# Kernel optimization log

Hardware: AMD Instinct MI355X
Metric: run time of the kernel (lower is better)

## Reference

```python
import jax, jax.numpy as jnp
import numpy as np
import math

D_MODEL = 1024
NUM_HEADS = 16
HEAD_DIM = D_MODEL // NUM_HEADS
B, L = 4, 1024


def setup_inputs() -> dict:
    key = jax.random.key(0)
    ks = jax.random.split(key, 14)
    s = 1.0 / math.sqrt(D_MODEL)
    return {
        "q": jax.random.normal(ks[0], (B, L, D_MODEL), jnp.float32),
        "k": jax.random.normal(ks[1], (B, L, D_MODEL), jnp.float32),
        "v": jax.random.normal(ks[2], (B, L, D_MODEL), jnp.float32),
        "Wq": jax.random.normal(ks[3], (D_MODEL, D_MODEL), jnp.float32) * s,
        "bq": jnp.zeros((D_MODEL,), jnp.float32),
        "Wk": jax.random.normal(ks[4], (D_MODEL, D_MODEL), jnp.float32) * s,
        "bk": jnp.zeros((D_MODEL,), jnp.float32),
        "Wv": jax.random.normal(ks[5], (D_MODEL, D_MODEL), jnp.float32) * s,
        "bv": jnp.zeros((D_MODEL,), jnp.float32),
        "Wo": jax.random.normal(ks[6], (D_MODEL, D_MODEL), jnp.float32) * s,
        "bo": jnp.zeros((D_MODEL,), jnp.float32),
        "lambda_q": jax.random.normal(ks[7], (HEAD_DIM,), jnp.float32) * 0.1,
        "lambda_k": jax.random.normal(ks[8], (HEAD_DIM,), jnp.float32) * 0.1,
        "lambda_v": jax.random.normal(ks[9], (HEAD_DIM,), jnp.float32) * 0.1,
    }


def reference(q, k, v, Wq, bq, Wk, bk, Wv, bv, Wo, bo, lambda_q, lambda_k, lambda_v):
    Bq, Lq, _ = q.shape
    # projections (torch Linear: x @ W.T + b)
    def split_heads(x):
        return x.reshape(Bq, -1, NUM_HEADS, HEAD_DIM).transpose(0, 2, 1, 3)  # [B,H,L,hd]
    qh = split_heads(q @ Wq.T + bq)
    kh = split_heads(k @ Wk.T + bk)
    vh = split_heads(v @ Wv.T + bv)

    lam_self = jnp.exp(jnp.sum(lambda_q * lambda_k))
    lam_cross = jnp.exp(jnp.sum(lambda_k * lambda_v))
    scale = 1.0 / math.sqrt(HEAD_DIM)

    scores_self = jnp.einsum('bhld,bhmd->bhlm', kh, vh) * scale   # [B,H,Lk,Lk]
    scores_cross = jnp.einsum('bhld,bhmd->bhlm', qh, kh) * scale  # [B,H,Lq,Lk]
    scores = scores_cross * lam_cross + scores_self * lam_self

    attn_weights = jax.nn.softmax(jnp.nan_to_num(scores, nan=0.0), axis=-1)
    attn_out = jnp.einsum('bhlm,bhmd->bhld', attn_weights, vh)
    attn_out = attn_out.transpose(0, 2, 1, 3).reshape(Bq, Lq, D_MODEL)
    out = attn_out @ Wo.T + bo
    return (out, attn_weights)
```

## Files before the change

### kernel.cpp

```cpp
#include <hip/hip_runtime.h>
#include <math.h>

#define D_MODEL 1024
#define NHEADS  16
#define HD      64
#define BSZ     4
#define LSEQ    1024
#define BH      64

typedef _Float16 f16;
typedef _Float16 f16x8 __attribute__((ext_vector_type(8)));
typedef _Float16 f16x4 __attribute__((ext_vector_type(4)));
typedef float    f32x4 __attribute__((ext_vector_type(4)));

typedef const __attribute__((address_space(1))) void* gp1_t;
typedef __attribute__((address_space(3))) void* lp3_t;

__device__ __forceinline__ void gload_lds16(const void* g, void* l) {
    __builtin_amdgcn_global_load_lds((gp1_t)g, (lp3_t)l, 16, 0, 0);
}

__global__ void lam_kernel(const float* __restrict__ lq, const float* __restrict__ lk,
                           const float* __restrict__ lv, float* __restrict__ lam) {
    int t = threadIdx.x;
    float pc = lk[t] * lv[t];
    float ps = lq[t] * lk[t];
#pragma unroll
    for (int o = 32; o > 0; o >>= 1) {
        pc += __shfl_down(pc, o, 64);
        ps += __shfl_down(ps, o, 64);
    }
    if (t == 0) {
        float lamC = expf(pc), lamS = expf(ps);
        lam[0] = lamC; lam[1] = lamS;
        lam[2] = lamC / lamS;
        lam[3] = 0.125f * lamS;
    }
}

__global__ void cvt_f32_f16_kernel(const float* __restrict__ src, f16* __restrict__ dst, int n8) {
    int i = blockIdx.x * blockDim.x + threadIdx.x;
    if (i < n8) {
        float4 a = *(const float4*)(src + (size_t)i * 8);
        float4 b = *(const float4*)(src + (size_t)i * 8 + 4);
        f16x8 h;
        h[0]=(f16)a.x; h[1]=(f16)a.y; h[2]=(f16)a.z; h[3]=(f16)a.w;
        h[4]=(f16)b.x; h[5]=(f16)b.y; h[6]=(f16)b.z; h[7]=(f16)b.w;
        *(f16x8*)(dst + (size_t)i * 8) = h;
    }
}

template<int AMODE, int OMODE>
__global__ __launch_bounds__(256) void gemm16_kernel(
    const void* __restrict__ Aarg, const f16* __restrict__ B16,
    const float* __restrict__ bias, const float* __restrict__ lam,
    void* __restrict__ Yarg)
{
    __shared__ f16 At[128 * 64];
    __shared__ f16 Btl[128 * 64];

    const int t = threadIdx.x;
    const int lane = t & 63, w = t >> 6;
    const int g = lane >> 4, ln = lane & 15;
    const int wr = w >> 1, wc = w & 1;
    const int n0 = blockIdx.x * 128, m0 = blockIdx.y * 128;

    f32x4 acc[4][4];
#pragma unroll
    for (int mi = 0; mi < 4; ++mi)
#pragma unroll
        for (int ni = 0; ni < 4; ++ni)
            acc[mi][ni] = (f32x4){0.f, 0.f, 0.f, 0.f};

    for (int kt = 0; kt < 16; ++kt) {
        if (AMODE == 0) {
            const float* X = (const float*)Aarg;
            int r = t >> 1, k0 = (t & 1) * 32;
            const float* src = X + (size_t)(m0 + r) * 1024 + kt * 64 + k0;
#pragma unroll
            for (int c = 0; c < 4; ++c) {
                float4 f0 = *(const float4*)(src + c * 8);
                float4 f1 = *(const float4*)(src + c * 8 + 4);
                f16x8 hv;
                hv[0]=(f16)f0.x; hv[1]=(f16)f0.y; hv[2]=(f16)f0.z; hv[3]=(f16)f0.w;
                hv[4]=(f16)f1.x; hv[5]=(f16)f1.y; hv[6]=(f16)f1.z; hv[7]=(f16)f1.w;
                int kb = (k0 + c * 8) * 2;
                *(f16x8*)((char*)At + r * 128 + (kb ^ ((r & 7) << 4))) = hv;
            }
        } else {
            const f16* A16 = (const f16*)Aarg;
#pragma unroll
            for (int i = 0; i < 4; ++i) {
                int o = t * 16 + i * 4096;
                int r = o >> 7, kb = (o & 127) ^ ((r & 7) << 4);
                gload_lds16(A16 + (size_t)(m0 + r) * 1024 + kt * 64 + (kb >> 1), (char*)At + o);
            }
        }
#pragma unroll
        for (int i = 0; i < 4; ++i) {
            int o = t * 16 + i * 4096;
            int r = o >> 7, kb = (o & 127) ^ ((r & 7) << 4);
            gload_lds16(B16 + (size_t)(n0 + r) * 1024 + kt * 64 + (kb >> 1), (char*)Btl + o);
        }
        __syncthreads();
#pragma unroll
        for (int ks = 0; ks < 2; ++ks) {
            f16x8 af[4], bf[4];
#pragma unroll
            for (int mi = 0; mi < 4; ++mi) {
                int r = wr * 64 + mi * 16 + ln;
                af[mi] = *(const f16x8*)((const char*)At + r * 128 + ((ks * 64 + g * 16) ^ ((r & 7) << 4)));
            }
#pragma unroll
            for (int ni = 0; ni < 4; ++ni) {
                int r = wc * 64 + ni * 16 + ln;
                bf[ni] = *(const f16x8*)((const char*)Btl + r * 128 + ((ks * 64 + g * 16) ^ ((r & 7) << 4)));
            }
#pragma unroll
            for (int mi = 0; mi < 4; ++mi)
#pragma unroll
                for (int ni = 0; ni < 4; ++ni)
                    acc[mi][ni] = __builtin_amdgcn_mfma_f32_16x16x32_f16(af[mi], bf[ni], acc[mi][ni], 0, 0, 0);
        }
        __syncthreads();
    }

    float alpha = 1.0f;
    if (OMODE == 1) alpha = lam[2];
#pragma unroll
    for (int mi = 0; mi < 4; ++mi) {
#pragma unroll
        for (int ni = 0; ni < 4; ++ni) {
            int n = n0 + wc * 64 + ni * 16 + ln;
            float bn = bias[n];
#pragma unroll
            for (int q = 0; q < 4; ++q) {
                int m = m0 + wr * 64 + mi * 16 + 4 * g + q;
                float v = acc[mi][ni][q] + bn;
                if (OMODE == 0) {
                    ((float*)Yarg)[(size_t)m * 1024 + n] = v;
                } else {
                    v *= alpha;
                    int b = m >> 10, l = m & 1023;
                    int h = n >> 6, d = n & 63;
                    ((f16*)Yarg)[(((size_t)(b * NHEADS + h)) * LSEQ + l) * HD + d] = (f16)v;
                }
            }
        }
    }
}

__global__ __launch_bounds__(256) void vtrans_kernel(const f16* __restrict__ Vh, f16* __restrict__ Vt) {
    __shared__ f16 tile[64 * 72];
    int t = threadIdx.x;
    int cb = blockIdx.x;
    int bh = blockIdx.y;
    size_t base = (size_t)bh * LSEQ * HD;
    {
        int c = t >> 2, d0 = (t & 3) * 16;
        f16x8 v0 = *(const f16x8*)(Vh + base + (size_t)(cb * 64 + c) * HD + d0);
        f16x8 v1 = *(const f16x8*)(Vh + base + (size_t)(cb * 64 + c) * HD + d0 + 8);
        *(f16x8*)((char*)tile + c * 144 + d0 * 2) = v0;
        *(f16x8*)((char*)tile + c * 144 + d0 * 2 + 16) = v1;
    }
    __syncthreads();
    {
        int d = t >> 2, c0 = (t & 3) * 16;
        f16 buf[16];
#pragma unroll
        for (int j = 0; j < 16; ++j)
            buf[j] = *(const f16*)((const char*)tile + (c0 + j) * 144 + d * 2);
        f16x8 o0, o1;
#pragma unroll
        for (int j = 0; j < 8; ++j) { o0[j] = buf[j]; o1[j] = buf[j + 8]; }
        size_t ob = (size_t)bh * HD * LSEQ + (size_t)d * LSEQ + cb * 64 + c0;
        *(f16x8*)(Vt + ob) = o0;
        *(f16x8*)(Vt + ob + 8) = o1;
    }
}

__global__ __launch_bounds__(256) void attn_kernel(
    const f16* __restrict__ Qs, const f16* __restrict__ Kh, const f16* __restrict__ Vh,
    const f16* __restrict__ Vt, const float* __restrict__ lam,
    float* __restrict__ attnW, f16* __restrict__ AO)
{
    __shared__ f16 Qt[64 * 128];
    __shared__ f16 Bt[64 * 128];
    __shared__ f16 Vts[64 * 64];
    __shared__ f16 Ws[64 * 72];
    __shared__ float linv[64];

    const int t = threadIdx.x;
    const int lane = t & 63;
    const int w = t >> 6;
    const int g = lane >> 4;
    const int ln = lane & 15;
    const int rb = blockIdx.x;
    const int bh = blockIdx.y;
    const size_t hbase = (size_t)bh * LSEQ * HD;
    const float gamma = lam[3];

    {
        const int r0 = rb * 64;
#pragma unroll
        for (int i = 0; i < 4; ++i) {
            int o = t * 16 + i * 4096;
            int r = o >> 8, kb = (o & 255) ^ ((r & 7) << 4);
            const f16* src = (kb < 128) ? (Qs + hbase + (size_t)(r0 + r) * HD + (kb >> 1))
                                        : (Kh + hbase + (size_t)(r0 + r) * HD + ((kb - 128) >> 1));
            gload_lds16(src, (char*)Qt + o);
        }
    }
    __syncthreads();

    f16x8 qf[4];
    {
        int r = w * 16 + ln;
#pragma unroll
        for (int ks = 0; ks < 4; ++ks)
            qf[ks] = *(const f16x8*)((const char*)Qt + r * 256 + ((ks * 64 + g * 16) ^ ((r & 7) << 4)));
    }

    float lsum = 0.f;
    for (int tt = 0; tt < 16; ++tt) {
        {
            const int c0 = tt * 64;
#pragma unroll
            for (int i = 0; i < 4; ++i) {
                int o = t * 16 + i * 4096;
                int r = o >> 8, kb = (o & 255) ^ ((r & 7) << 4);
                const f16* src = (kb < 128) ? (Kh + hbase + (size_t)(c0 + r) * HD + (kb >> 1))
                                            : (Vh + hbase + (size_t)(c0 + r) * HD + ((kb - 128) >> 1));
                gload_lds16(src, (char*)Bt + o);
            }
        }
        __syncthreads();
#pragma unroll
        for (int ci = 0; ci < 4; ++ci) {
            f32x4 acc = (f32x4){0.f, 0.f, 0.f, 0.f};
#pragma unroll
            for (int ks = 0; ks < 4; ++ks) {
                int c = ci * 16 + ln;
                f16x8 af = *(const f16x8*)((const char*)Bt + c * 256 + ((ks * 64 + g * 16) ^ ((c & 7) << 4)));
                acc = __builtin_amdgcn_mfma_f32_16x16x32_f16(af, qf[ks], acc, 0, 0, 0);
            }
#pragma unroll
            for (int q = 0; q < 4; ++q) lsum += __expf(acc[q] * gamma);
        }
        __syncthreads();
    }
    lsum += __shfl_xor(lsum, 16, 64);
    lsum += __shfl_xor(lsum, 32, 64);
    if (g == 0) linv[w * 16 + ln] = 1.0f / lsum;
    __syncthreads();

    f32x4 oacc[4];
#pragma unroll
    for (int dj = 0; dj < 4; ++dj) oacc[dj] = (f32x4){0.f, 0.f, 0.f, 0.f};

    for (int tt = 0; tt < 16; ++tt) {
        {
            const int c0 = tt * 64;
#pragma unroll
            for (int i = 0; i < 4; ++i) {
                int o = t * 16 + i * 4096;
                int r = o >> 8, kb = (o & 255) ^ ((r & 7) << 4);
                const f16* src = (kb < 128) ? (Kh + hbase + (size_t)(c0 + r) * HD + (kb >> 1))
                                            : (Vh + hbase + (size_t)(c0 + r) * HD + ((kb - 128) >> 1));
                gload_lds16(src, (char*)Bt + o);
            }
#pragma unroll
            for (int i = 0; i < 2; ++i) {
                int o = t * 16 + i * 4096;
                int r = o >> 7, kb = (o & 127) ^ ((r & 7) << 4);
                const f16* src = Vt + (size_t)bh * HD * LSEQ + (size_t)r * LSEQ + tt * 64 + (kb >> 1);
                gload_lds16(src, (char*)Vts + o);
            }
        }
        __syncthreads();

        {
            int r = w * 16 + ln;
            float il = linv[r];
#pragma unroll
            for (int ci = 0; ci < 4; ++ci) {
                f32x4 acc = (f32x4){0.f, 0.f, 0.f, 0.f};
#pragma unroll
                for (int ks = 0; ks < 4; ++ks) {
                    int c = ci * 16 + ln;
                    f16x8 af = *(const f16x8*)((const char*)Bt + c * 256 + ((ks * 64 + g * 16) ^ ((c & 7) << 4)));
                    acc = __builtin_amdgcn_mfma_f32_16x16x32_f16(af, qf[ks], acc, 0, 0, 0);
                }
                float4 wv;
                wv.x = __expf(acc[0] * gamma) * il;
                wv.y = __expf(acc[1] * gamma) * il;
                wv.z = __expf(acc[2] * gamma) * il;
                wv.w = __expf(acc[3] * gamma) * il;
                size_t gi = (((size_t)bh * LSEQ) + rb * 64 + r) * LSEQ + tt * 64 + ci * 16 + 4 * g;
                *(float4*)(attnW + gi) = wv;
                f16x4 wh;
                wh[0] = (f16)wv.x; wh[1] = (f16)wv.y; wh[2] = (f16)wv.z; wh[3] = (f16)wv.w;
                *(f16x4*)((char*)Ws + r * 144 + ci * 32 + g * 8) = wh;
            }
        }
#pragma unroll
        for (int ks = 0; ks < 2; ++ks) {
            int r = w * 16 + ln;
            f16x8 pa = *(const f16x8*)((const char*)Ws + r * 144 + ks * 64 + g * 16);
#pragma unroll
            for (int dj = 0; dj < 4; ++dj) {
                int d = dj * 16 + ln;
                f16x8 vb = *(const f16x8*)((const char*)Vts + d * 128 + ((ks * 64 + g * 16) ^ ((d & 7) << 4)));
                oacc[dj] = __builtin_amdgcn_mfma_f32_16x16x32_f16(pa, vb, oacc[dj], 0, 0, 0);
            }
        }
        __syncthreads();
    }

    {
        const int b = bh >> 4, h = bh & 15;
#pragma unroll
        for (int dj = 0; dj < 4; ++dj)
#pragma unroll
            for (int q = 0; q < 4; ++q) {
                int l = rb * 64 + w * 16 + 4 * g + q;
                int col = h * 64 + dj * 16 + ln;
                AO[((size_t)b * LSEQ + l) * D_MODEL + col] = (f16)oacc[dj][q];
            }
    }
}

extern "C" void kernel_launch(void* const* d_in, const int* in_sizes, int n_in,
                              void* d_out, int out_size, void* d_ws, size_t ws_size,
                              hipStream_t stream) {
    const float* q  = (const float*)d_in[0];
    const float* k  = (const float*)d_in[1];
    const float* v  = (const float*)d_in[2];
    const float* Wq = (const float*)d_in[3];
    const float* bq = (const float*)d_in[4];
    const float* Wk = (const float*)d_in[5];
    const float* bk = (const float*)d_in[6];
    const float* Wv = (const float*)d_in[7];
    const float* bv = (const float*)d_in[8];
    const float* Wo = (const float*)d_in[9];
    const float* bo = (const float*)d_in[10];
    const float* lq = (const float*)d_in[11];
    const float* lk = (const float*)d_in[12];
    const float* lv = (const float*)d_in[13];

    float* out   = (float*)d_out;
    float* attnW = out + (size_t)BSZ * LSEQ * D_MODEL;

    f16* ws16 = (f16*)d_ws;
    const size_t HSZ = (size_t)BH * LSEQ * HD;
    f16* Qs   = ws16;
    f16* Kh   = ws16 + HSZ;
    f16* Vh   = ws16 + 2 * HSZ;
    f16* Vt   = ws16 + 3 * HSZ;
    f16* AO   = ws16 + 4 * HSZ;
    f16* W16q = ws16 + 5 * HSZ;
    f16* W16k = W16q + 1048576;
    f16* W16v = W16k + 1048576;
    f16* W16o = W16v + 1048576;
    float* lam = (float*)(W16o + 1048576);

    lam_kernel<<<1, 64, 0, stream>>>(lq, lk, lv, lam);

    cvt_f32_f16_kernel<<<512, 256, 0, stream>>>(Wq, W16q, 131072);
    cvt_f32_f16_kernel<<<512, 256, 0, stream>>>(Wk, W16k, 131072);
    cvt_f32_f16_kernel<<<512, 256, 0, stream>>>(Wv, W16v, 131072);
    cvt_f32_f16_kernel<<<512, 256, 0, stream>>>(Wo, W16o, 131072);

    dim3 ggrid(8, 32);
    gemm16_kernel<0, 1><<<ggrid, 256, 0, stream>>>((const void*)q, W16q, bq, lam, (void*)Qs);
    gemm16_kernel<0, 2><<<ggrid, 256, 0, stream>>>((const void*)k, W16k, bk, lam, (void*)Kh);
    gemm16_kernel<0, 2><<<ggrid, 256, 0, stream>>>((const void*)v, W16v, bv, lam, (void*)Vh);

    vtrans_kernel<<<dim3(16, 64), 256, 0, stream>>>(Vh, Vt);

    attn_kernel<<<dim3(16, 64), 256, 0, stream>>>(Qs, Kh, Vh, Vt, lam, attnW, AO);

    gemm16_kernel<1, 0><<<ggrid, 256, 0, stream>>>((const void*)AO, W16o, bo, lam, (void*)out);
}
```

Measured before the change: 296.1 us.

## Batch weight casts and QKV GEMMs, double-buffer loads, fuse V transpose

Merges the four weight conversion launches into one, and the three QKV projection GEMMs into one launch over a z-dimension. It adds double-buffered LDS prefetch to both GEMMs, and writes the transposed V directly from the GEMM epilogue, which removes the separate transpose kernel. The attention kernel now processes 128 rows per block with 512 threads, double-buffers K/V and Vt tiles, and remaps block ids so neighbouring blocks share heads. It also writes attention weights with nontemporal stores. In exchange it uses more LDS per block, which may reduce occupancy.

```diff
diff --git a/kernel.cpp b/kernel.cpp
--- a/kernel.cpp
+++ b/kernel.cpp
@@ -38,32 +38,43 @@
     }
 }
 
-__global__ void cvt_f32_f16_kernel(const float* __restrict__ src, f16* __restrict__ dst, int n8) {
+__global__ __launch_bounds__(256) void cvt4_kernel(
+    const float* __restrict__ s0, const float* __restrict__ s1,
+    const float* __restrict__ s2, const float* __restrict__ s3,
+    f16* __restrict__ d0, f16* __restrict__ d1, f16* __restrict__ d2, f16* __restrict__ d3) {
+    int which = blockIdx.y;
+    const float* src = which == 0 ? s0 : which == 1 ? s1 : which == 2 ? s2 : s3;
+    f16* dst = which == 0 ? d0 : which == 1 ? d1 : which == 2 ? d2 : d3;
     int i = blockIdx.x * blockDim.x + threadIdx.x;
-    if (i < n8) {
-        float4 a = *(const float4*)(src + (size_t)i * 8);
-        float4 b = *(const float4*)(src + (size_t)i * 8 + 4);
-        f16x8 h;
-        h[0]=(f16)a.x; h[1]=(f16)a.y; h[2]=(f16)a.z; h[3]=(f16)a.w;
-        h[4]=(f16)b.x; h[5]=(f16)b.y; h[6]=(f16)b.z; h[7]=(f16)b.w;
-        *(f16x8*)(dst + (size_t)i * 8) = h;
-    }
-}
-
-template<int AMODE, int OMODE>
-__global__ __launch_bounds__(256) void gemm16_kernel(
-    const void* __restrict__ Aarg, const f16* __restrict__ B16,
-    const float* __restrict__ bias, const float* __restrict__ lam,
-    void* __restrict__ Yarg)
+    float4 a = *(const float4*)(src + (size_t)i * 8);
+    float4 b = *(const float4*)(src + (size_t)i * 8 + 4);
+    f16x8 h;
+    h[0]=(f16)a.x; h[1]=(f16)a.y; h[2]=(f16)a.z; h[3]=(f16)a.w;
+    h[4]=(f16)b.x; h[5]=(f16)b.y; h[6]=(f16)b.z; h[7]=(f16)b.w;
+    *(f16x8*)(dst + (size_t)i * 8) = h;
+}
+
+__global__ __launch_bounds__(256, 2) void gemm_qkv_kernel(
+    const float* __restrict__ q, const float* __restrict__ k, const float* __restrict__ v,
+    const f16* __restrict__ Wq, const f16* __restrict__ Wk, const f16* __restrict__ Wv,
+    const float* __restrict__ bq, const float* __restrict__ bk, const float* __restrict__ bv,
+    const float* __restrict__ lam,
+    f16* __restrict__ Qs, f16* __restrict__ Kh, f16* __restrict__ Vh, f16* __restrict__ Vt)
 {
-    __shared__ f16 At[128 * 64];
-    __shared__ f16 Btl[128 * 64];
+    __shared__ f16 At[2][128 * 64];
+    __shared__ f16 Bt[2][128 * 64];
+
+    const int z = blockIdx.z;
+    const float* X    = (z == 0) ? q  : (z == 1) ? k  : v;
+    const f16*   W    = (z == 0) ? Wq : (z == 1) ? Wk : Wv;
+    const float* bias = (z == 0) ? bq : (z == 1) ? bk : bv;
 
     const int t = threadIdx.x;
     const int lane = t & 63, w = t >> 6;
     const int g = lane >> 4, ln = lane & 15;
     const int wr = w >> 1, wc = w & 1;
     const int n0 = blockIdx.x * 128, m0 = blockIdx.y * 128;
+    const int ar = t >> 1, ak = (t & 1) * 32;
 
     f32x4 acc[4][4];
 #pragma unroll
@@ -72,49 +83,153 @@
         for (int ni = 0; ni < 4; ++ni)
             acc[mi][ni] = (f32x4){0.f, 0.f, 0.f, 0.f};
 
+    {
+        const float* src = X + (size_t)(m0 + ar) * 1024 + ak;
+#pragma unroll
+        for (int c = 0; c < 4; ++c) {
+            float4 f0 = ((const float4*)src)[c * 2];
+            float4 f1 = ((const float4*)src)[c * 2 + 1];
+            f16x8 hv;
+            hv[0]=(f16)f0.x; hv[1]=(f16)f0.y; hv[2]=(f16)f0.z; hv[3]=(f16)f0.w;
+            hv[4]=(f16)f1.x; hv[5]=(f16)f1.y; hv[6]=(f16)f1.z; hv[7]=(f16)f1.w;
+            int kb = (ak + c * 8) * 2;
+            *(f16x8*)((char*)At[0] + ar * 128 + (kb ^ ((ar & 7) << 4))) = hv;
+        }
+#pragma unroll
+        for (int i = 0; i < 4; ++i) {
+            int o = t * 16 + i * 4096;
+            int r = o >> 7, kb = (o & 127) ^ ((r & 7) << 4);
+            gload_lds16(W + (size_t)(n0 + r) * 1024 + (kb >> 1), (char*)Bt[0] + o);
+        }
+    }
+    __syncthreads();
+
+    int cur = 0;
     for (int kt = 0; kt < 16; ++kt) {
-        if (AMODE == 0) {
-            const float* X = (const float*)Aarg;
-            int r = t >> 1, k0 = (t & 1) * 32;
-            const float* src = X + (size_t)(m0 + r) * 1024 + kt * 64 + k0;
+        float4 pre[8];
+        if (kt < 15) {
+            const float* src = X + (size_t)(m0 + ar) * 1024 + (kt + 1) * 64 + ak;
+#pragma unroll
+            for (int c = 0; c < 8; ++c) pre[c] = ((const float4*)src)[c];
+#pragma unroll
+            for (int i = 0; i < 4; ++i) {
+                int o = t * 16 + i * 4096;
+                int r = o >> 7, kb = (o & 127) ^ ((r & 7) << 4);
+                gload_lds16(W + (size_t)(n0 + r) * 1024 + (kt + 1) * 64 + (kb >> 1),
+                            (char*)Bt[cur ^ 1] + o);
+            }
+        }
+#pragma unroll
+        for (int ks = 0; ks < 2; ++ks) {
+            f16x8 af[4], bf[4];
+#pragma unroll
+            for (int mi = 0; mi < 4; ++mi) {
+                int r = wr * 64 + mi * 16 + ln;
+                af[mi] = *(const f16x8*)((const char*)At[cur] + r * 128 + ((ks * 64 + g * 16) ^ ((r & 7) << 4)));
+            }
+#pragma unroll
+            for (int ni = 0; ni < 4; ++ni) {
+                int r = wc * 64 + ni * 16 + ln;
+                bf[ni] = *(const f16x8*)((const char*)Bt[cur] + r * 128 + ((ks * 64 + g * 16) ^ ((r & 7) << 4)));
+            }
+#pragma unroll
+            for (int mi = 0; mi < 4; ++mi)
+#pragma unroll
+                for (int ni = 0; ni < 4; ++ni)
+                    acc[mi][ni] = __builtin_amdgcn_mfma_f32_16x16x32_f16(af[mi], bf[ni], acc[mi][ni], 0, 0, 0);
+        }
+        if (kt < 15) {
 #pragma unroll
             for (int c = 0; c < 4; ++c) {
-                float4 f0 = *(const float4*)(src + c * 8);
-                float4 f1 = *(const float4*)(src + c * 8 + 4);
+                float4 f0 = pre[c * 2], f1 = pre[c * 2 + 1];
                 f16x8 hv;
                 hv[0]=(f16)f0.x; hv[1]=(f16)f0.y; hv[2]=(f16)f0.z; hv[3]=(f16)f0.w;
                 hv[4]=(f16)f1.x; hv[5]=(f16)f1.y; hv[6]=(f16)f1.z; hv[7]=(f16)f1.w;
-                int kb = (k0 + c * 8) * 2;
-                *(f16x8*)((char*)At + r * 128 + (kb ^ ((r & 7) << 4))) = hv;
-            }
-        } else {
-            const f16* A16 = (const f16*)Aarg;
+                int kb = (ak + c * 8) * 2;
+                *(f16x8*)((char*)At[cur ^ 1] + ar * 128 + (kb ^ ((ar & 7) << 4))) = hv;
+            }
+        }
+        __syncthreads();
+        cur ^= 1;
+    }
+
+    const float alpha = (z == 0) ? lam[2] : 1.0f;
+    f16* Y = (z == 0) ? Qs : (z == 1) ? Kh : Vh;
+#pragma unroll
+    for (int mi = 0; mi < 4; ++mi) {
+#pragma unroll
+        for (int ni = 0; ni < 4; ++ni) {
+            int n = n0 + wc * 64 + ni * 16 + ln;
+            int h = n >> 6, d = n & 63;
+            float bn = bias[n];
+            int mrow0 = m0 + wr * 64 + mi * 16 + 4 * g;
+            int b = mrow0 >> 10, l0 = mrow0 & 1023;
+            f16x4 tv;
+#pragma unroll
+            for (int qq = 0; qq < 4; ++qq) {
+                float val = (acc[mi][ni][qq] + bn) * alpha;
+                f16 hq = (f16)val;
+                tv[qq] = hq;
+                Y[(((size_t)(b * NHEADS + h)) * LSEQ + l0 + qq) * HD + d] = hq;
+            }
+            if (z == 2)
+                *(f16x4*)(Vt + ((size_t)(b * NHEADS + h) * HD + d) * LSEQ + l0) = tv;
+        }
+    }
+}
+
+__global__ __launch_bounds__(256, 2) void gemm_ao_kernel(
+    const f16* __restrict__ A16, const f16* __restrict__ W16,
+    const float* __restrict__ bias, float* __restrict__ out)
+{
+    __shared__ f16 At[2][128 * 64];
+    __shared__ f16 Bt[2][128 * 64];
+
+    const int t = threadIdx.x;
+    const int lane = t & 63, w = t >> 6;
+    const int g = lane >> 4, ln = lane & 15;
+    const int wr = w >> 1, wc = w & 1;
+    const int n0 = blockIdx.x * 128, m0 = blockIdx.y * 128;
+
+    f32x4 acc[4][4];
+#pragma unroll
+    for (int mi = 0; mi < 4; ++mi)
+#pragma unroll
+        for (int ni = 0; ni < 4; ++ni)
+            acc[mi][ni] = (f32x4){0.f, 0.f, 0.f, 0.f};
+
+#pragma unroll
+    for (int i = 0; i < 4; ++i) {
+        int o = t * 16 + i * 4096;
+        int r = o >> 7, kb = (o & 127) ^ ((r & 7) << 4);
+        gload_lds16(A16 + (size_t)(m0 + r) * 1024 + (kb >> 1), (char*)At[0] + o);
+        gload_lds16(W16 + (size_t)(n0 + r) * 1024 + (kb >> 1), (char*)Bt[0] + o);
+    }
+    __syncthreads();
+
+    int cur = 0;
+    for (int kt = 0; kt < 16; ++kt) {
+        if (kt < 15) {
 #pragma unroll
             for (int i = 0; i < 4; ++i) {
                 int o = t * 16 + i * 4096;
                 int r = o >> 7, kb = (o & 127) ^ ((r & 7) << 4);
-                gload_lds16(A16 + (size_t)(m0 + r) * 1024 + kt * 64 + (kb >> 1), (char*)At + o);
-            }
-        }
-#pragma unroll
-        for (int i = 0; i < 4; ++i) {
-            int o = t * 16 + i * 4096;
-            int r = o >> 7, kb = (o & 127) ^ ((r & 7) << 4);
-            gload_lds16(B16 + (size_t)(n0 + r) * 1024 + kt * 64 + (kb >> 1), (char*)Btl + o);
-        }
-        __syncthreads();
+                gload_lds16(A16 + (size_t)(m0 + r) * 1024 + (kt + 1) * 64 + (kb >> 1), (char*)At[cur ^ 1] + o);
+                gload_lds16(W16 + (size_t)(n0 + r) * 1024 + (kt + 1) * 64 + (kb >> 1), (char*)Bt[cur ^ 1] + o);
+            }
+        }
 #pragma unroll
         for (int ks = 0; ks < 2; ++ks) {
             f16x8 af[4], bf[4];
 #pragma unroll
             for (int mi = 0; mi < 4; ++mi) {
                 int r = wr * 64 + mi * 16 + ln;
-                af[mi] = *(const f16x8*)((const char*)At + r * 128 + ((ks * 64 + g * 16) ^ ((r & 7) << 4)));
+                af[mi] = *(const f16x8*)((const char*)At[cur] + r * 128 + ((ks * 64 + g * 16) ^ ((r & 7) << 4)));
             }
 #pragma unroll
             for (int ni = 0; ni < 4; ++ni) {
                 int r = wc * 64 + ni * 16 + ln;
-                bf[ni] = *(const f16x8*)((const char*)Btl + r * 128 + ((ks * 64 + g * 16) ^ ((r & 7) << 4)));
+                bf[ni] = *(const f16x8*)((const char*)Bt[cur] + r * 128 + ((ks * 64 + g * 16) ^ ((r & 7) << 4)));
             }
 #pragma unroll
             for (int mi = 0; mi < 4; ++mi)
@@ -123,93 +238,61 @@
                     acc[mi][ni] = __builtin_amdgcn_mfma_f32_16x16x32_f16(af[mi], bf[ni], acc[mi][ni], 0, 0, 0);
         }
         __syncthreads();
-    }
-
-    float alpha = 1.0f;
-    if (OMODE == 1) alpha = lam[2];
-#pragma unroll
-    for (int mi = 0; mi < 4; ++mi) {
+        cur ^= 1;
+    }
+
+#pragma unroll
+    for (int mi = 0; mi < 4; ++mi)
 #pragma unroll
         for (int ni = 0; ni < 4; ++ni) {
             int n = n0 + wc * 64 + ni * 16 + ln;
             float bn = bias[n];
 #pragma unroll
-            for (int q = 0; q < 4; ++q) {
-                int m = m0 + wr * 64 + mi * 16 + 4 * g + q;
-                float v = acc[mi][ni][q] + bn;
-                if (OMODE == 0) {
-                    ((float*)Yarg)[(size_t)m * 1024 + n] = v;
-                } else {
-                    v *= alpha;
-                    int b = m >> 10, l = m & 1023;
-                    int h = n >> 6, d = n & 63;
-                    ((f16*)Yarg)[(((size_t)(b * NHEADS + h)) * LSEQ + l) * HD + d] = (f16)v;
-                }
-            }
-        }
-    }
-}
-
-__global__ __launch_bounds__(256) void vtrans_kernel(const f16* __restrict__ Vh, f16* __restrict__ Vt) {
-    __shared__ f16 tile[64 * 72];
-    int t = threadIdx.x;
-    int cb = blockIdx.x;
-    int bh = blockIdx.y;
-    size_t base = (size_t)bh * LSEQ * HD;
-    {
-        int c = t >> 2, d0 = (t & 3) * 16;
-        f16x8 v0 = *(const f16x8*)(Vh + base + (size_t)(cb * 64 + c) * HD + d0);
-        f16x8 v1 = *(const f16x8*)(Vh + base + (size_t)(cb * 64 + c) * HD + d0 + 8);
-        *(f16x8*)((char*)tile + c * 144 + d0 * 2) = v0;
-        *(f16x8*)((char*)tile + c * 144 + d0 * 2 + 16) = v1;
-    }
-    __syncthreads();
-    {
-        int d = t >> 2, c0 = (t & 3) * 16;
-        f16 buf[16];
-#pragma unroll
-        for (int j = 0; j < 16; ++j)
-            buf[j] = *(const f16*)((const char*)tile + (c0 + j) * 144 + d * 2);
-        f16x8 o0, o1;
-#pragma unroll
-        for (int j = 0; j < 8; ++j) { o0[j] = buf[j]; o1[j] = buf[j + 8]; }
-        size_t ob = (size_t)bh * HD * LSEQ + (size_t)d * LSEQ + cb * 64 + c0;
-        *(f16x8*)(Vt + ob) = o0;
-        *(f16x8*)(Vt + ob + 8) = o1;
-    }
-}
-
-__global__ __launch_bounds__(256) void attn_kernel(
+            for (int qq = 0; qq < 4; ++qq) {
+                int m = m0 + wr * 64 + mi * 16 + 4 * g + qq;
+                out[(size_t)m * 1024 + n] = acc[mi][ni][qq] + bn;
+            }
+        }
+}
+
+__global__ __launch_bounds__(512, 4) void attn_kernel(
     const f16* __restrict__ Qs, const f16* __restrict__ Kh, const f16* __restrict__ Vh,
     const f16* __restrict__ Vt, const float* __restrict__ lam,
     float* __restrict__ attnW, f16* __restrict__ AO)
 {
-    __shared__ f16 Qt[64 * 128];
-    __shared__ f16 Bt[64 * 128];
-    __shared__ f16 Vts[64 * 64];
-    __shared__ f16 Ws[64 * 72];
-    __shared__ float linv[64];
+    __shared__ char smem[81920];
+    char* QtWs = smem;
+    char* BtB  = smem + 32768;
+    char* VtsB = smem + 65536;
 
     const int t = threadIdx.x;
-    const int lane = t & 63;
-    const int w = t >> 6;
-    const int g = lane >> 4;
-    const int ln = lane & 15;
-    const int rb = blockIdx.x;
-    const int bh = blockIdx.y;
+    const int lane = t & 63, w = t >> 6;
+    const int g = lane >> 4, ln = lane & 15;
+
+    const int bid = blockIdx.x;
+    const int wg = (bid & 7) * 64 + (bid >> 3);
+    const int bh = wg >> 3, rb = wg & 7;
     const size_t hbase = (size_t)bh * LSEQ * HD;
     const float gamma = lam[3];
 
     {
-        const int r0 = rb * 64;
+        const int r0 = rb * 128;
 #pragma unroll
         for (int i = 0; i < 4; ++i) {
-            int o = t * 16 + i * 4096;
+            int o = t * 16 + i * 8192;
             int r = o >> 8, kb = (o & 255) ^ ((r & 7) << 4);
             const f16* src = (kb < 128) ? (Qs + hbase + (size_t)(r0 + r) * HD + (kb >> 1))
                                         : (Kh + hbase + (size_t)(r0 + r) * HD + ((kb - 128) >> 1));
-            gload_lds16(src, (char*)Qt + o);
-        }
+            gload_lds16(src, QtWs + o);
+        }
+    }
+#pragma unroll
+    for (int i = 0; i < 2; ++i) {
+        int o = t * 16 + i * 8192;
+        int r = o >> 8, kb = (o & 255) ^ ((r & 7) << 4);
+        const f16* src = (kb < 128) ? (Kh + hbase + (size_t)r * HD + (kb >> 1))
+                                    : (Vh + hbase + (size_t)r * HD + ((kb - 128) >> 1));
+        gload_lds16(src, BtB + o);
     }
     __syncthreads();
 
@@ -218,103 +301,106 @@
         int r = w * 16 + ln;
 #pragma unroll
         for (int ks = 0; ks < 4; ++ks)
-            qf[ks] = *(const f16x8*)((const char*)Qt + r * 256 + ((ks * 64 + g * 16) ^ ((r & 7) << 4)));
+            qf[ks] = *(const f16x8*)(QtWs + r * 256 + ((ks * 64 + g * 16) ^ ((r & 7) << 4)));
     }
 
     float lsum = 0.f;
+    int cur = 0;
     for (int tt = 0; tt < 16; ++tt) {
         {
-            const int c0 = tt * 64;
-#pragma unroll
-            for (int i = 0; i < 4; ++i) {
-                int o = t * 16 + i * 4096;
+            const int c0 = ((tt + 1) & 15) * 64;
+#pragma unroll
+            for (int i = 0; i < 2; ++i) {
+                int o = t * 16 + i * 8192;
                 int r = o >> 8, kb = (o & 255) ^ ((r & 7) << 4);
                 const f16* src = (kb < 128) ? (Kh + hbase + (size_t)(c0 + r) * HD + (kb >> 1))
                                             : (Vh + hbase + (size_t)(c0 + r) * HD + ((kb - 128) >> 1));
-                gload_lds16(src, (char*)Bt + o);
-            }
-        }
-        __syncthreads();
+                gload_lds16(src, BtB + (cur ^ 1) * 16384 + o);
+            }
+            if (tt == 15) {
+                int o = t * 16;
+                int d = o >> 7, kb = (o & 127) ^ ((d & 7) << 4);
+                gload_lds16(Vt + (size_t)bh * HD * LSEQ + (size_t)d * LSEQ + (kb >> 1),
+                            VtsB + (cur ^ 1) * 8192 + o);
+            }
+        }
 #pragma unroll
         for (int ci = 0; ci < 4; ++ci) {
             f32x4 acc = (f32x4){0.f, 0.f, 0.f, 0.f};
 #pragma unroll
             for (int ks = 0; ks < 4; ++ks) {
                 int c = ci * 16 + ln;
-                f16x8 af = *(const f16x8*)((const char*)Bt + c * 256 + ((ks * 64 + g * 16) ^ ((c & 7) << 4)));
+                f16x8 af = *(const f16x8*)(BtB + cur * 16384 + c * 256 + ((ks * 64 + g * 16) ^ ((c & 7) << 4)));
                 acc = __builtin_amdgcn_mfma_f32_16x16x32_f16(af, qf[ks], acc, 0, 0, 0);
             }
 #pragma unroll
-            for (int q = 0; q < 4; ++q) lsum += __expf(acc[q] * gamma);
+            for (int qq = 0; qq < 4; ++qq) lsum += __expf(acc[qq] * gamma);
         }
         __syncthreads();
+        cur ^= 1;
     }
     lsum += __shfl_xor(lsum, 16, 64);
     lsum += __shfl_xor(lsum, 32, 64);
-    if (g == 0) linv[w * 16 + ln] = 1.0f / lsum;
-    __syncthreads();
+    const float il = 1.0f / lsum;
 
     f32x4 oacc[4];
 #pragma unroll
     for (int dj = 0; dj < 4; ++dj) oacc[dj] = (f32x4){0.f, 0.f, 0.f, 0.f};
 
     for (int tt = 0; tt < 16; ++tt) {
-        {
-            const int c0 = tt * 64;
-#pragma unroll
-            for (int i = 0; i < 4; ++i) {
-                int o = t * 16 + i * 4096;
+        if (tt < 15) {
+            const int c0 = (tt + 1) * 64;
+#pragma unroll
+            for (int i = 0; i < 2; ++i) {
+                int o = t * 16 + i * 8192;
                 int r = o >> 8, kb = (o & 255) ^ ((r & 7) << 4);
                 const f16* src = (kb < 128) ? (Kh + hbase + (size_t)(c0 + r) * HD + (kb >> 1))
                                             : (Vh + hbase + (size_t)(c0 + r) * HD + ((kb - 128) >> 1));
-                gload_lds16(src, (char*)Bt + o);
-            }
-#pragma unroll
-            for (int i = 0; i < 2; ++i) {
-                int o = t * 16 + i * 4096;
-                int r = o >> 7, kb = (o & 127) ^ ((r & 7) << 4);
-                const f16* src = Vt + (size_t)bh * HD * LSEQ + (size_t)r * LSEQ + tt * 64 + (kb >> 1);
-                gload_lds16(src, (char*)Vts + o);
-            }
-        }
-        __syncthreads();
-
+                gload_lds16(src, BtB + (cur ^ 1) * 16384 + o);
+            }
+            {
+                int o = t * 16;
+                int d = o >> 7, kb = (o & 127) ^ ((d & 7) << 4);
+                gload_lds16(Vt + (size_t)bh * HD * LSEQ + (size_t)d * LSEQ + c0 + (kb >> 1),
+                            VtsB + (cur ^ 1) * 8192 + o);
+            }
+        }
         {
-            int r = w * 16 + ln;
-            float il = linv[r];
+            const int r = w * 16 + ln;
 #pragma unroll
             for (int ci = 0; ci < 4; ++ci) {
                 f32x4 acc = (f32x4){0.f, 0.f, 0.f, 0.f};
 #pragma unroll
                 for (int ks = 0; ks < 4; ++ks) {
                     int c = ci * 16 + ln;
-                    f16x8 af = *(const f16x8*)((const char*)Bt + c * 256 + ((ks * 64 + g * 16) ^ ((c & 7) << 4)));
+                    f16x8 af = *(const f16x8*)(BtB + cur * 16384 + c * 256 + ((ks * 64 + g * 16) ^ ((c & 7) << 4)));
                     acc = __builtin_amdgcn_mfma_f32_16x16x32_f16(af, qf[ks], acc, 0, 0, 0);
                 }
-                float4 wv;
-                wv.x = __expf(acc[0] * gamma) * il;
-                wv.y = __expf(acc[1] * gamma) * il;
-                wv.z = __expf(acc[2] * gamma) * il;
-                wv.w = __expf(acc[3] * gamma) * il;
-                size_t gi = (((size_t)bh * LSEQ) + rb * 64 + r) * LSEQ + tt * 64 + ci * 16 + 4 * g;
-                *(float4*)(attnW + gi) = wv;
+                f32x4 wv;
+                wv[0] = __expf(acc[0] * gamma) * il;
+                wv[1] = __expf(acc[1] * gamma) * il;
+                wv[2] = __expf(acc[2] * gamma) * il;
+                wv[3] = __expf(acc[3] * gamma) * il;
+                size_t gi = ((size_t)bh * LSEQ + rb * 128 + r) * LSEQ + tt * 64 + ci * 16 + 4 * g;
+                __builtin_nontemporal_store(wv, (f32x4*)(attnW + gi));
                 f16x4 wh;
-                wh[0] = (f16)wv.x; wh[1] = (f16)wv.y; wh[2] = (f16)wv.z; wh[3] = (f16)wv.w;
-                *(f16x4*)((char*)Ws + r * 144 + ci * 32 + g * 8) = wh;
+                wh[0] = (f16)wv[0]; wh[1] = (f16)wv[1]; wh[2] = (f16)wv[2]; wh[3] = (f16)wv[3];
+                *(f16x4*)(QtWs + r * 144 + ci * 32 + g * 8) = wh;
             }
         }
 #pragma unroll
         for (int ks = 0; ks < 2; ++ks) {
             int r = w * 16 + ln;
-            f16x8 pa = *(const f16x8*)((const char*)Ws + r * 144 + ks * 64 + g * 16);
+            f16x8 pa = *(const f16x8*)(QtWs + r * 144 + ks * 64 + g * 16);
 #pragma unroll
             for (int dj = 0; dj < 4; ++dj) {
                 int d = dj * 16 + ln;
-                f16x8 vb = *(const f16x8*)((const char*)Vts + d * 128 + ((ks * 64 + g * 16) ^ ((d & 7) << 4)));
+                f16x8 vb = *(const f16x8*)(VtsB + cur * 8192 + d * 128 + ((ks * 64 + g * 16) ^ ((d & 7) << 4)));
                 oacc[dj] = __builtin_amdgcn_mfma_f32_16x16x32_f16(pa, vb, oacc[dj], 0, 0, 0);
             }
         }
         __syncthreads();
+        cur ^= 1;
     }
 
     {
@@ -322,10 +408,9 @@
 #pragma unroll
         for (int dj = 0; dj < 4; ++dj)
 #pragma unroll
-            for (int q = 0; q < 4; ++q) {
-                int l = rb * 64 + w * 16 + 4 * g + q;
-                int col = h * 64 + dj * 16 + ln;
-                AO[((size_t)b * LSEQ + l) * D_MODEL + col] = (f16)oacc[dj][q];
+            for (int qq = 0; qq < 4; ++qq) {
+                int l = rb * 128 + w * 16 + 4 * g + qq;
+                AO[((size_t)b * LSEQ + l) * D_MODEL + h * 64 + dj * 16 + ln] = (f16)oacc[dj][qq];
             }
     }
 }
@@ -366,19 +451,12 @@
 
     lam_kernel<<<1, 64, 0, stream>>>(lq, lk, lv, lam);
 
-    cvt_f32_f16_kernel<<<512, 256, 0, stream>>>(Wq, W16q, 131072);
-    cvt_f32_f16_kernel<<<512, 256, 0, stream>>>(Wk, W16k, 131072);
-    cvt_f32_f16_kernel<<<512, 256, 0, stream>>>(Wv, W16v, 131072);
-    cvt_f32_f16_kernel<<<512, 256, 0, stream>>>(Wo, W16o, 131072);
-
-    dim3 ggrid(8, 32);
-    gemm16_kernel<0, 1><<<ggrid, 256, 0, stream>>>((const void*)q, W16q, bq, lam, (void*)Qs);
-    gemm16_kernel<0, 2><<<ggrid, 256, 0, stream>>>((const void*)k, W16k, bk, lam, (void*)Kh);
-    gemm16_kernel<0, 2><<<ggrid, 256, 0, stream>>>((const void*)v, W16v, bv, lam, (void*)Vh);
-
-    vtrans_kernel<<<dim3(16, 64), 256, 0, stream>>>(Vh, Vt);
-
-    attn_kernel<<<dim3(16, 64), 256, 0, stream>>>(Qs, Kh, Vh, Vt, lam, attnW, AO);
-
-    gemm16_kernel<1, 0><<<ggrid, 256, 0, stream>>>((const void*)AO, W16o, bo, lam, (void*)out);
-}
+    cvt4_kernel<<<dim3(512, 4), 256, 0, stream>>>(Wq, Wk, Wv, Wo, W16q, W16k, W16v, W16o);
+
+    gemm_qkv_kernel<<<dim3(8, 32, 3), 256, 0, stream>>>(
+        q, k, v, W16q, W16k, W16v, bq, bk, bv, lam, Qs, Kh, Vh, Vt);
+
+    attn_kernel<<<512, 512, 0, stream>>>(Qs, Kh, Vh, Vt, lam, attnW, AO);
+
+    gemm_ao_kernel<<<dim3(8, 32), 256, 0, stream>>>(AO, W16o, bo, out);
+}
```

Measured after the change: 247.7 us. 1.2x faster.
